# Performance work log

Measured on AMD Instinct MI355X. Metric: run time of the kernel, lower is better.

Reference implementation:

```python
import jax, jax.numpy as jnp
import numpy as np

EPS = 1e-5


def causal_conv(x, w, b):
    # x: [B,C,N,T], w: [O,C,K] (temporal kernel), b: [O]; left-pad time by K-1 (causal)
    K = w.shape[-1]
    y = jax.lax.conv_general_dilated(
        x, w[:, :, None, :], window_strides=(1, 1),
        padding=[(0, 0), (K - 1, 0)],
        dimension_numbers=('NCHW', 'OIHW', 'NCHW'))
    return y + b[None, :, None, None]


def batchnorm(x, gamma, beta):
    # training-mode BatchNorm2d: stats over (B, N, T) per channel
    m = x.mean(axis=(0, 2, 3), keepdims=True)
    v = x.var(axis=(0, 2, 3), keepdims=True)
    return (x - m) * jax.lax.rsqrt(v + EPS) * gamma[None, :, None, None] + beta[None, :, None, None]


def st_layer(x, supports, gamma, beta, rw, rb, aw, ab, gw, gb, ow, ob):
    # residual 1x1 conv
    res = jnp.einsum('bcnt,oc->bont', x, rw) + rb[None, :, None, None]
    x = jax.nn.relu(batchnorm(x, gamma, beta))
    aff = causal_conv(x, aw, ab)
    gate = causal_conv(x, gw, gb)
    x = jnp.tanh(aff + res) * jax.nn.sigmoid(gate)
    B, C, N, T = x.shape
    hs = jnp.einsum('bcvt,evw->becwt', x, supports)  # [B,E,C,N,T]
    full = jnp.concatenate([x, hs.reshape(B, -1, N, T)], axis=1)  # [B,C*(E+1),N,T]
    return jnp.einsum('bcnt,oc->bont', full, ow) + ob[None, :, None, None]


def reference(x, supports, bn_gamma, bn_beta, res_w, res_b, aff_w, aff_b,
              gate_w, gate_b, gc_w, gc_b, attn_w1, attn_b1, attn_w2, attn_b2,
              attn_w3, attn_b3):
    L = bn_gamma.shape[0]
    h = x
    stack = [x]
    for i in range(L):
        h = st_layer(h, supports, bn_gamma[i], bn_beta[i], res_w[i], res_b[i],
                     aff_w[i], aff_b[i], gate_w[i], gate_b[i], gc_w[i], gc_b[i])
        stack.append(h)
    xs = jax.nn.relu(jnp.stack(stack, axis=2))  # [B,C,L+1,N,T]
    # SelfAttention: 1x1x1 conv3d chain C->64->64->1 with ReLU after first two
    e = jax.nn.relu(jnp.einsum('bclnt,oc->bolnt', xs, attn_w1) + attn_b1[None, :, None, None, None])
    e = jax.nn.relu(jnp.einsum('bclnt,oc->bolnt', e, attn_w2) + attn_b2[None, :, None, None, None])
    e = jnp.einsum('bclnt,oc->bolnt', e, attn_w3) + attn_b3[None, :, None, None, None]  # [B,1,L+1,N,T]
    w = jax.nn.softmax(e, axis=2)
    out = (xs * w).sum(axis=2)  # [B,C,N,T]
    return out


def setup_inputs() -> dict:
    B, C, N, T = 16, 32, 500, 64
    L, E, K, D = 4, 2, 3, 64
    key = jax.random.key(0)
    ks = jax.random.split(key, 20)
    s = 0.1
    return {
        'x': jax.random.normal(ks[0], (B, C, N, T), jnp.float32),
        'supports': jax.random.uniform(ks[1], (E, N, N), jnp.float32) / N,
        'bn_gamma': jnp.ones((L, C), jnp.float32),
        'bn_beta': jnp.zeros((L, C), jnp.float32),
        'res_w': jax.random.normal(ks[2], (L, C, C), jnp.float32) * s,
        'res_b': jax.random.normal(ks[3], (L, C), jnp.float32) * s,
        'aff_w': jax.random.normal(ks[4], (L, C, C, K), jnp.float32) * s,
        'aff_b': jax.random.normal(ks[5], (L, C), jnp.float32) * s,
        'gate_w': jax.random.normal(ks[6], (L, C, C, K), jnp.float32) * s,
        'gate_b': jax.random.normal(ks[7], (L, C), jnp.float32) * s,
        'gc_w': jax.random.normal(ks[8], (L, C, C * (E + 1)), jnp.float32) * s,
        'gc_b': jax.random.normal(ks[9], (L, C), jnp.float32) * s,
        'attn_w1': jax.random.normal(ks[10], (D, C), jnp.float32) * s,
        'attn_b1': jax.random.normal(ks[11], (D,), jnp.float32) * s,
        'attn_w2': jax.random.normal(ks[12], (D, D), jnp.float32) * s,
        'attn_b2': jax.random.normal(ks[13], (D,), jnp.float32) * s,
        'attn_w3': jax.random.normal(ks[14], (1, D), jnp.float32) * s,
        'attn_b3': jax.random.normal(ks[15], (1,), jnp.float32) * s,
    }
```

## Files before the change

### kernel.cpp

```cpp
#include <hip/hip_runtime.h>
#include <hip/hip_bf16.h>
#include <math.h>

#define B_ 16
#define C_ 32
#define N_ 500
#define T_ 64
#define L_ 4
#define BSTR (C_*N_*T_)
#define CSTR (N_*T_)
#define TENS ((size_t)B_*C_*N_*T_)
#define CNT_ 512000.0

typedef short s8v __attribute__((ext_vector_type(8)));
typedef float f4v __attribute__((ext_vector_type(4)));
typedef unsigned short u16;

__global__ __launch_bounds__(256) void zero_kernel(double* __restrict__ p,
                                                   float* __restrict__ slack) {
  p[threadIdx.x] = 0.0;
  if (threadIdx.x < 16) slack[threadIdx.x] = 0.f;
}

__global__ __launch_bounds__(256) void stats_kernel(const float* __restrict__ h,
                                                    double* __restrict__ st) {
  int c = blockIdx.x, b = blockIdx.y, tid = threadIdx.x;
  const float4* p = (const float4*)(h + (size_t)b*BSTR + (size_t)c*CSTR);
  double s = 0.0, s2 = 0.0;
  for (int i = tid; i < CSTR/4; i += 256) {
    float4 v = p[i];
    s  += (double)v.x + (double)v.y + (double)v.z + (double)v.w;
    s2 += (double)v.x*v.x + (double)v.y*v.y + (double)v.z*v.z + (double)v.w*v.w;
  }
  __shared__ double sd[256], sd2[256];
  sd[tid] = s; sd2[tid] = s2; __syncthreads();
  for (int off = 128; off > 0; off >>= 1) {
    if (tid < off) { sd[tid] += sd[tid+off]; sd2[tid] += sd2[tid+off]; }
    __syncthreads();
  }
  if (tid == 0) { atomicAdd(&st[2*c], sd[0]); atomicAdd(&st[2*c+1], sd2[0]); }
}

__global__ __launch_bounds__(256) void aconv_kernel(const float* __restrict__ sup,
                                                    short* __restrict__ ATh) {
  int idx = blockIdx.x*256 + threadIdx.x;
  int k = idx & 1023, w = idx >> 10;
  float val = 0.f;
  if (k < 1000 && w < N_) {
    int s = k >= 500;
    int v = k - s*500;
    val = sup[((size_t)s*N_ + v)*N_ + w];
  }
  __hip_bfloat16 bh = __float2bfloat16(val);
  ATh[idx] = *(short*)&bh;
}

__global__ __launch_bounds__(256) void w1t_kernel(const float* __restrict__ W1,
                                                  float* __restrict__ W1T) {
  int idx = blockIdx.x*256 + threadIdx.x;
  int c = idx >> 6, k = idx & 63;
  W1T[c*64 + k] = W1[k*32 + c];
}

__global__ __launch_bounds__(256) void wprep_kernel(
    const float* __restrict__ aw, const float* __restrict__ gw,
    const float* __restrict__ rw,
    u16* __restrict__ wagh, u16* __restrict__ wagl,
    u16* __restrict__ wrh,  u16* __restrict__ wrl)
{
  int idx = blockIdx.x*256 + threadIdx.x;
  if (idx >= 28672) return;
  float v; u16 *dh, *dl; int di;
  if (idx < 24576) {
    int l = idx / 6144, r = idx % 6144;
    int tap = r / 2048, col = (r >> 5) & 63, c = r & 31;
    v = (col < 32) ? aw[l*3072 + (col*32 + c)*3 + tap]
                   : gw[l*3072 + ((col-32)*32 + c)*3 + tap];
    dh = wagh; dl = wagl; di = idx;
  } else {
    int j = idx - 24576;
    int l = j >> 10, o = (j >> 5) & 31, c = j & 31;
    v = rw[l*1024 + o*32 + c];
    dh = wrh; dl = wrl; di = j;
  }
  __hip_bfloat16 bh = __float2bfloat16(v);
  float fh = __bfloat162float(bh);
  __hip_bfloat16 bl = __float2bfloat16(v - fh);
  dh[di] = *(u16*)&bh;
  dl[di] = *(u16*)&bl;
}

__global__ __launch_bounds__(512) void fuse4_kernel(
    const float* __restrict__ h, const double* __restrict__ st,
    const float* __restrict__ gamma, const float* __restrict__ beta,
    const u16* __restrict__ wagh, const u16* __restrict__ wagl,
    const u16* __restrict__ wrh,  const u16* __restrict__ wrl,
    const float* __restrict__ rb, const float* __restrict__ ab,
    const float* __restrict__ gb,
    const float* __restrict__ gcw, const float* __restrict__ gcb,
    float* __restrict__ Y0, u16* __restrict__ Y1h, u16* __restrict__ Y2h)
{
  __shared__ __align__(16) char smem[41600];
  __shared__ float ssc[C_], ssb[C_];
  u16* Sxh = (u16*)smem;
  u16* Sxl = Sxh + 5280;
  u16* Shh = Sxl + 5280;
  u16* Shl = Shh + 5120;
  float* Sz = (float*)smem;

  int tid = threadIdx.x;
  int bx  = blockIdx.x;
  int b = bx / 250, np = bx - b*250;
  size_t off0 = (size_t)b*BSTR + (size_t)(np*2)*T_;

  int m  = tid & 127;
  int c0 = (tid >> 7) << 3;
  float hv[8];
  #pragma unroll
  for (int j = 0; j < 8; j++)
    hv[j] = h[off0 + (size_t)(c0 + j)*CSTR + m];

  if (tid < C_) {
    double mm = st[2*tid] * (1.0/CNT_);
    double vv = st[2*tid+1] * (1.0/CNT_) - mm*mm;
    float sc = gamma[tid] * (float)(1.0 / sqrt(vv + 1e-5));
    ssc[tid] = sc;
    ssb[tid] = beta[tid] - (float)mm * sc;
  }
  __syncthreads();

  union P { u16 s[8]; int4 v; };
  P hh8, hl8, xh8, xl8;
  #pragma unroll
  for (int j = 0; j < 8; j++) {
    float hval = hv[j];
    __hip_bfloat16 t1 = __float2bfloat16(hval);
    hh8.s[j] = *(u16*)&t1;
    __hip_bfloat16 t2 = __float2bfloat16(hval - __bfloat162float(t1));
    hl8.s[j] = *(u16*)&t2;
    float xval = fmaxf(fmaf(hval, ssc[c0+j], ssb[c0+j]), 0.f);
    __hip_bfloat16 t3 = __float2bfloat16(xval);
    xh8.s[j] = *(u16*)&t3;
    __hip_bfloat16 t4 = __float2bfloat16(xval - __bfloat162float(t3));
    xl8.s[j] = *(u16*)&t4;
  }
  *(int4*)&Shh[m*40 + c0] = hh8.v;
  *(int4*)&Shl[m*40 + c0] = hl8.v;
  int xrow = m + 2 + (m >> 6)*2;
  *(int4*)&Sxh[xrow*40 + c0] = xh8.v;
  *(int4*)&Sxl[xrow*40 + c0] = xl8.v;
  if (tid < 32) {
    int pl = tid >> 4, rsel = (tid >> 2) & 3, ch = tid & 3;
    int row = (rsel & 1) + (rsel >> 1)*66;
    int4 z4 = {0,0,0,0};
    *(int4*)((pl ? Sxl : Sxh) + row*40 + ch*8) = z4;
  }
  __syncthreads();

  int lane = tid & 63;
  int wave = __builtin_amdgcn_readfirstlane(tid >> 6);
  int node = wave >> 2, t0 = (wave & 3) << 4;
  int l15 = lane & 15, q = lane >> 4;

  f4v affc[2], gatec[2], resc[2];
  #pragma unroll
  for (int i = 0; i < 2; i++) {
    affc[i] = (f4v){0.f,0.f,0.f,0.f};
    gatec[i] = (f4v){0.f,0.f,0.f,0.f};
    resc[i] = (f4v){0.f,0.f,0.f,0.f};
  }

  {
    int ha = (node*64 + t0 + l15)*40 + q*8;
    s8v hhf = *(const s8v*)&Shh[ha];
    s8v hlf = *(const s8v*)&Shl[ha];
    #pragma unroll
    for (int ct = 0; ct < 2; ct++) {
      int wb = (ct*16 + l15)*32 + q*8;
      s8v wh = *(const s8v*)&wrh[wb];
      s8v wl = *(const s8v*)&wrl[wb];
      f4v d = resc[ct];
      d = __builtin_amdgcn_mfma_f32_16x16x32_bf16(hhf, wh, d, 0, 0, 0);
      d = __builtin_amdgcn_mfma_f32_16x16x32_bf16(hlf, wh, d, 0, 0, 0);
      d = __builtin_amdgcn_mfma_f32_16x16x32_bf16(hhf, wl, d, 0, 0, 0);
      resc[ct] = d;
    }
  }
  #pragma unroll
  for (int tap = 0; tap < 3; tap++) {
    int xa = (node*66 + t0 + l15 + tap)*40 + q*8;
    s8v xhf = *(const s8v*)&Sxh[xa];
    s8v xlf = *(const s8v*)&Sxl[xa];
    #pragma unroll
    for (int ct = 0; ct < 4; ct++) {
      int wb = (tap*64 + ct*16 + l15)*32 + q*8;
      s8v wh = *(const s8v*)&wagh[wb];
      s8v wl = *(const s8v*)&wagl[wb];
      f4v d = (ct < 2) ? affc[ct] : gatec[ct-2];
      d = __builtin_amdgcn_mfma_f32_16x16x32_bf16(xhf, wh, d, 0, 0, 0);
      d = __builtin_amdgcn_mfma_f32_16x16x32_bf16(xlf, wh, d, 0, 0, 0);
      d = __builtin_amdgcn_mfma_f32_16x16x32_bf16(xhf, wl, d, 0, 0, 0);
      if (ct < 2) affc[ct] = d; else gatec[ct-2] = d;
    }
  }
  __syncthreads();

  #pragma unroll
  for (int ct = 0; ct < 2; ct++) {
    int o = ct*16 + l15;
    float abias = ab[o] + rb[o];
    float gbias = gb[o];
    #pragma unroll
    for (int r = 0; r < 4; r++) {
      float a = affc[ct][r] + resc[ct][r] + abias;
      float g = gatec[ct][r] + gbias;
      float z = tanhf(a) * (1.f/(1.f + expf(-g)));
      Sz[node*2080 + o*65 + (t0 + q*4 + r)] = z;
    }
  }
  __syncthreads();

  int t = tid & 63;
  int og = wave;
  float y0a[2][4] = {}, y1a[2][4] = {}, y2a[2][4] = {};
  for (int c = 0; c < C_; c++) {
    float g0[4], g1[4], g2[4];
    #pragma unroll
    for (int jq = 0; jq < 4; jq++) {
      const float* gr = gcw + (og*4 + jq)*96;
      g0[jq] = gr[c]; g1[jq] = gr[32 + c]; g2[jq] = gr[64 + c];
    }
    #pragma unroll
    for (int nn = 0; nn < 2; nn++) {
      float zc = Sz[nn*2080 + c*65 + t];
      #pragma unroll
      for (int jq = 0; jq < 4; jq++) {
        y0a[nn][jq] = fmaf(g0[jq], zc, y0a[nn][jq]);
        y1a[nn][jq] = fmaf(g1[jq], zc, y1a[nn][jq]);
        y2a[nn][jq] = fmaf(g2[jq], zc, y2a[nn][jq]);
      }
    }
  }
  #pragma unroll
  for (int nn = 0; nn < 2; nn++)
    #pragma unroll
    for (int jq = 0; jq < 4; jq++) {
      int oo = og*4 + jq;
      size_t pp = off0 + (size_t)nn*T_ + (size_t)oo*CSTR + t;
      Y0[pp] = y0a[nn][jq] + gcb[oo];
      __hip_bfloat16 b1 = __float2bfloat16(y1a[nn][jq]);
      __hip_bfloat16 b2 = __float2bfloat16(y2a[nn][jq]);
      Y1h[pp] = *(u16*)&b1;
      Y2h[pp] = *(u16*)&b2;
    }
}

__global__ __launch_bounds__(256) void trans_kernel(
    const u16* __restrict__ Y1h, const u16* __restrict__ Y2h,
    u16* __restrict__ Yt)
{
  __shared__ u16 S[64*68];
  int bx = blockIdx.x;
  int o = bx & 31, vg = bx >> 5;
  int b = blockIdx.y;
  int tid = threadIdx.x;
  u16* dst = Yt + (size_t)(b*C_ + o)*64000;
  for (int ic = 0; ic < 4; ic++) {
    int vc = vg*4 + ic;
    __syncthreads();
    #pragma unroll
    for (int i = 0; i < 2; i++) {
      int vrow = (tid >> 3) + i*32;
      int vv = vc*64 + vrow;
      int t8 = (tid & 7)*8;
      int4 val = {0,0,0,0};
      if (vv < 1000) {
        int sup = vv >= 500;
        int n = vv - sup*500;
        const u16* src = (sup ? Y2h : Y1h) + (size_t)b*BSTR + (size_t)o*CSTR
                         + (size_t)n*T_;
        val = *(const int4*)(src + t8);
      }
      *(int4*)&S[vrow*68 + t8] = val;
    }
    __syncthreads();
    int t2 = tid >> 3, vs = tid & 7;
    if (vc < 15 || vs < 5) {
      unsigned r[8];
      #pragma unroll
      for (int j = 0; j < 8; j++)
        r[j] = *(const unsigned*)&S[(vs*8 + j)*68 + 2*t2];
      u16 lo[8], hi[8];
      #pragma unroll
      for (int j = 0; j < 8; j++) { lo[j] = (u16)r[j]; hi[j] = (u16)(r[j] >> 16); }
      *(int4*)(dst + (size_t)(2*t2)*1000   + vc*64 + vs*8) = *(const int4*)lo;
      *(int4*)(dst + (size_t)(2*t2+1)*1000 + vc*64 + vs*8) = *(const int4*)hi;
    }
  }
}

__global__ __launch_bounds__(256) void diff6_kernel(
    const u16* __restrict__ Yt,
    const short* __restrict__ ATh,
    float* __restrict__ out, double* __restrict__ stp)
{
  __shared__ short Asd[64*40];
  __shared__ short Bsd[128*40];

  int tid = threadIdx.x;
  int bx = blockIdx.x;
  int mtile = bx & 15, wtile = bx >> 4;
  int b = blockIdx.y;
  int w0 = wtile << 6;

  int lane = tid & 63;
  int wave = __builtin_amdgcn_readfirstlane(tid >> 6);
  int wi = wave & 1, wj = wave >> 1;
  int l15 = lane & 15, quad = lane >> 4;
  int o = mtile*2 + wj;

  int offA[2], offB[4];
  #pragma unroll
  for (int ti = 0; ti < 2; ti++) offA[ti] = (wi*32 + ti*16 + l15)*40 + quad*8;
  #pragma unroll
  for (int tj = 0; tj < 4; tj++) offB[tj] = (wj*64 + tj*16 + l15)*40 + quad*8;

  int akq = tid & 3, awl = tid >> 2;
  const short* aSrc = ATh + (size_t)(w0 + awl)*1024 + akq*8;
  short* aDst = &Asd[awl*40 + akq*8];
  const u16* bSrc[2]; short* bDst[2];
  #pragma unroll
  for (int i = 0; i < 2; i++) {
    int idx = tid + i*256;
    int kq = idx & 3, m = idx >> 2;
    int oo = m >> 6, tl = m & 63;
    bSrc[i] = Yt + ((size_t)(b*C_ + mtile*2 + oo)*64 + tl)*1000 + kq*8;
    bDst[i] = &Bsd[m*40 + kq*8];
  }

  f4v acc[8];
  #pragma unroll
  for (int i = 0; i < 8; i++) acc[i] = (f4v){0.f, 0.f, 0.f, 0.f};

  for (int k0 = 0; k0 < 1024; k0 += 32) {
    __syncthreads();
    *(int4*)aDst    = *(const int4*)(aSrc    + k0);
    *(int4*)bDst[0] = *(const int4*)(bSrc[0] + k0);
    *(int4*)bDst[1] = *(const int4*)(bSrc[1] + k0);
    __syncthreads();
    s8v bv[4];
    #pragma unroll
    for (int tj = 0; tj < 4; tj++) bv[tj] = *(const s8v*)&Bsd[offB[tj]];
    #pragma unroll
    for (int ti = 0; ti < 2; ti++) {
      s8v av = *(const s8v*)&Asd[offA[ti]];
      #pragma unroll
      for (int tj = 0; tj < 4; tj++)
        acc[ti*4+tj] = __builtin_amdgcn_mfma_f32_16x16x32_bf16(
                           av, bv[tj], acc[ti*4+tj], 0, 0, 0);
    }
  }

  float s = 0.f, s2 = 0.f;
  #pragma unroll
  for (int tj = 0; tj < 4; tj++) {
    int t = tj*16 + l15;
    float* obase = out + (((size_t)b*C_ + o)*N_)*T_ + t;
    #pragma unroll
    for (int ti = 0; ti < 2; ti++) {
      int wbase = w0 + wi*32 + ti*16 + quad*4;
      #pragma unroll
      for (int r = 0; r < 4; r++) {
        int w = wbase + r;
        if (w < N_) {
          float* p = obase + (size_t)w*T_;
          float val = *p + acc[ti*4+tj][r];
          *p = val;
          s += val;
          s2 = fmaf(val, val, s2);
        }
      }
    }
  }
  if (stp) {
    #pragma unroll
    for (int d = 32; d > 0; d >>= 1) {
      s  += __shfl_down(s,  d, 64);
      s2 += __shfl_down(s2, d, 64);
    }
    if (lane == 0) {
      atomicAdd(&stp[2*o],     (double)s);
      atomicAdd(&stp[2*o + 1], (double)s2);
    }
  }
}

__global__ __launch_bounds__(256) void attn3_kernel(
    const float* __restrict__ hsrc, float* __restrict__ O,
    float* __restrict__ sden,
    const float* __restrict__ W1T, const float* __restrict__ b1,
    const float* __restrict__ W2, const float* __restrict__ b2,
    const float* __restrict__ w3, const float* __restrict__ b3,
    int init)
{
  int tid = threadIdx.x;
  int t = tid & 63;
  int g = __builtin_amdgcn_readfirstlane(tid >> 6);
  int bx = blockIdx.x;
  int b = bx / 125;
  int n = (bx - b*125)*4 + g;
  size_t off = (size_t)b*BSTR + (size_t)n*T_;

  float h1r[64];
  #pragma unroll
  for (int k = 0; k < 64; k++) h1r[k] = b1[k];
  for (int c = 0; c < C_; c++) {
    float xv = fmaxf(hsrc[off + (size_t)c*CSTR + t], 0.f);
    const float* wr = W1T + c*64;
    #pragma unroll
    for (int k = 0; k < 64; k++) h1r[k] = fmaf(wr[k], xv, h1r[k]);
  }
  #pragma unroll
  for (int k = 0; k < 64; k++) h1r[k] = fmaxf(h1r[k], 0.f);

  float e = b3[0];
  for (int j = 0; j < 64; j++) {
    const float* w2r = W2 + j*64;
    float a0 = 0.f, a1 = 0.f, a2 = 0.f, a3 = 0.f;
    #pragma unroll
    for (int i = 0; i < 64; i += 4) {
      a0 = fmaf(w2r[i+0], h1r[i+0], a0);
      a1 = fmaf(w2r[i+1], h1r[i+1], a1);
      a2 = fmaf(w2r[i+2], h1r[i+2], a2);
      a3 = fmaf(w2r[i+3], h1r[i+3], a3);
    }
    float a = b2[j] + ((a0+a1)+(a2+a3));
    e = fmaf(w3[j], fmaxf(a, 0.f), e);
  }
  float p = expf(e);

  size_t si = (size_t)b*CSTR + (size_t)n*T_ + t;
  float so = init ? 0.f : sden[si];
  sden[si] = so + p;

  for (int c = 0; c < C_; c++) {
    size_t pi = off + (size_t)c*CSTR + t;
    float xv = fmaxf(hsrc[pi], 0.f);
    float ov = init ? 0.f : O[pi];
    O[pi] = fmaf(p, xv, ov);
  }
}

__global__ __launch_bounds__(256) void norm_kernel(float* __restrict__ O,
                                                   const float* __restrict__ sden) {
  unsigned idx = (blockIdx.x*256u + threadIdx.x) * 4u;
  unsigned b = idx / BSTR;
  unsigned r = idx - b*BSTR;
  unsigned nt = r % CSTR;
  float4 o = *(float4*)(O + idx);
  const float* sp = sden + (size_t)b*CSTR + nt;
  o.x /= sp[0]; o.y /= sp[1]; o.z /= sp[2]; o.w /= sp[3];
  *(float4*)(O + idx) = o;
}

extern "C" void kernel_launch(void* const* d_in, const int* in_sizes, int n_in,
                              void* d_out, int out_size, void* d_ws, size_t ws_size,
                              hipStream_t stream)
{
  const float* x    = (const float*)d_in[0];
  const float* sup  = (const float*)d_in[1];
  const float* bng  = (const float*)d_in[2];
  const float* bnb  = (const float*)d_in[3];
  const float* rw   = (const float*)d_in[4];
  const float* rb   = (const float*)d_in[5];
  const float* aw   = (const float*)d_in[6];
  const float* ab   = (const float*)d_in[7];
  const float* gw   = (const float*)d_in[8];
  const float* gb   = (const float*)d_in[9];
  const float* gcw  = (const float*)d_in[10];
  const float* gcb  = (const float*)d_in[11];
  const float* w1   = (const float*)d_in[12];
  const float* ab1  = (const float*)d_in[13];
  const float* w2   = (const float*)d_in[14];
  const float* ab2  = (const float*)d_in[15];
  const float* w3   = (const float*)d_in[16];
  const float* ab3  = (const float*)d_in[17];
  float* out = (float*)d_out;

  float* ws   = (float*)d_ws;
  float* bufA = ws;
  u16*   Y1h  = (u16*)(ws + TENS);
  u16*   Y2h  = Y1h + TENS;
  u16*   Yt   = (u16*)(ws + (size_t)2*TENS);
  float* slack= ws + (size_t)2*TENS + 16384000;
  float* sden = slack + 16;
  double* st  = (double*)(sden + (size_t)B_*N_*T_);
  short* ATh  = (short*)((float*)st + 1024);
  float* W1T  = (float*)(ATh + (size_t)512*1024);
  u16* WAGh = (u16*)(W1T + 2048);
  u16* WAGl = WAGh + 24576;
  u16* WRh  = WAGl + 24576;
  u16* WRl  = WRh + 4096;

  zero_kernel<<<1, 256, 0, stream>>>(st, slack);
  aconv_kernel<<<2048, 256, 0, stream>>>(sup, ATh);
  w1t_kernel<<<8, 256, 0, stream>>>(w1, W1T);
  wprep_kernel<<<112, 256, 0, stream>>>(aw, gw, rw, WAGh, WAGl, WRh, WRl);
  stats_kernel<<<dim3(C_, B_), 256, 0, stream>>>(x, st);
  attn3_kernel<<<B_*125, 256, 0, stream>>>(x, out, sden, W1T, ab1, w2, ab2, w3, ab3, 1);

  const float* hcur = x;
  for (int l = 0; l < L_; l++) {
    fuse4_kernel<<<B_*250, 512, 0, stream>>>(
        hcur, st + l*64, bng + l*C_, bnb + l*C_,
        WAGh + l*6144, WAGl + l*6144, WRh + l*1024, WRl + l*1024,
        rb + l*C_, ab + l*C_, gb + l*C_,
        gcw + l*C_*96, gcb + l*C_,
        bufA, Y1h, Y2h);
    trans_kernel<<<dim3(128, B_), 256, 0, stream>>>(Y1h, Y2h, Yt);
    diff6_kernel<<<dim3(128, B_), 256, 0, stream>>>(
        Yt, ATh, bufA, (l < L_-1) ? (st + (l+1)*64) : nullptr);
    attn3_kernel<<<B_*125, 256, 0, stream>>>(bufA, out, sden, W1T, ab1, w2, ab2, w3, ab3, 0);
    hcur = bufA;
  }
  norm_kernel<<<16000, 256, 0, stream>>>(out, sden);
}
```

Baseline: 1.638 ms.

## Move attention MLP onto bf16 MFMA with LDS staging

Rewrites the attention scoring kernel so the C->64->64 1x1 convolutions run as bf16 16x16x32 MFMA tiles. Activations are staged through LDS per wave instead of each thread holding a 64-float hidden vector and doing scalar FMAs. The activations are also kept in registers, so the second global read of the input for the weighted sum goes away. The weight prep kernel gains bf16 conversion of W1/W2 and replaces the transpose kernel. This trades fp32 precision in the attention logits for bf16 and relies on tensor-core throughput.

```diff
diff --git a/kernel.cpp b/kernel.cpp
--- a/kernel.cpp
+++ b/kernel.cpp
@@ -55,21 +55,27 @@
   ATh[idx] = *(short*)&bh;
 }
 
-__global__ __launch_bounds__(256) void w1t_kernel(const float* __restrict__ W1,
-                                                  float* __restrict__ W1T) {
-  int idx = blockIdx.x*256 + threadIdx.x;
-  int c = idx >> 6, k = idx & 63;
-  W1T[c*64 + k] = W1[k*32 + c];
-}
-
 __global__ __launch_bounds__(256) void wprep_kernel(
     const float* __restrict__ aw, const float* __restrict__ gw,
     const float* __restrict__ rw,
+    const float* __restrict__ w1, const float* __restrict__ w2,
     u16* __restrict__ wagh, u16* __restrict__ wagl,
-    u16* __restrict__ wrh,  u16* __restrict__ wrl)
+    u16* __restrict__ wrh,  u16* __restrict__ wrl,
+    u16* __restrict__ W1bf, u16* __restrict__ W2bf)
 {
   int idx = blockIdx.x*256 + threadIdx.x;
-  if (idx >= 28672) return;
+  if (idx >= 34816) return;
+  if (idx >= 28672) {
+    int j = idx - 28672;
+    if (j < 2048) {
+      __hip_bfloat16 bv = __float2bfloat16(w1[j]);
+      W1bf[j] = *(u16*)&bv;
+    } else {
+      __hip_bfloat16 bv = __float2bfloat16(w2[j - 2048]);
+      W2bf[j - 2048] = *(u16*)&bv;
+    }
+    return;
+  }
   float v; u16 *dh, *dl; int di;
   if (idx < 24576) {
     int l = idx / 6144, r = idx % 6144;
@@ -395,59 +401,122 @@
   }
 }
 
-__global__ __launch_bounds__(256) void attn3_kernel(
+__global__ __launch_bounds__(256) void attn4_kernel(
     const float* __restrict__ hsrc, float* __restrict__ O,
     float* __restrict__ sden,
-    const float* __restrict__ W1T, const float* __restrict__ b1,
-    const float* __restrict__ W2, const float* __restrict__ b2,
+    const u16* __restrict__ W1bf, const float* __restrict__ b1,
+    const u16* __restrict__ W2bf, const float* __restrict__ b2,
     const float* __restrict__ w3, const float* __restrict__ b3,
     int init)
 {
+  __shared__ u16 Sh[4*4608];
+  __shared__ float Se[4*64];
+
   int tid = threadIdx.x;
-  int t = tid & 63;
-  int g = __builtin_amdgcn_readfirstlane(tid >> 6);
+  int lane = tid & 63;
+  int wave = __builtin_amdgcn_readfirstlane(tid >> 6);
   int bx = blockIdx.x;
   int b = bx / 125;
-  int n = (bx - b*125)*4 + g;
+  int n = (bx - b*125)*4 + wave;
   size_t off = (size_t)b*BSTR + (size_t)n*T_;
-
-  float h1r[64];
-  #pragma unroll
-  for (int k = 0; k < 64; k++) h1r[k] = b1[k];
-  for (int c = 0; c < C_; c++) {
-    float xv = fmaxf(hsrc[off + (size_t)c*CSTR + t], 0.f);
-    const float* wr = W1T + c*64;
-    #pragma unroll
-    for (int k = 0; k < 64; k++) h1r[k] = fmaf(wr[k], xv, h1r[k]);
-  }
-  #pragma unroll
-  for (int k = 0; k < 64; k++) h1r[k] = fmaxf(h1r[k], 0.f);
-
-  float e = b3[0];
-  for (int j = 0; j < 64; j++) {
-    const float* w2r = W2 + j*64;
-    float a0 = 0.f, a1 = 0.f, a2 = 0.f, a3 = 0.f;
-    #pragma unroll
-    for (int i = 0; i < 64; i += 4) {
-      a0 = fmaf(w2r[i+0], h1r[i+0], a0);
-      a1 = fmaf(w2r[i+1], h1r[i+1], a1);
-      a2 = fmaf(w2r[i+2], h1r[i+2], a2);
-      a3 = fmaf(w2r[i+3], h1r[i+3], a3);
-    }
-    float a = b2[j] + ((a0+a1)+(a2+a3));
-    e = fmaf(w3[j], fmaxf(a, 0.f), e);
-  }
-  float p = expf(e);
-
-  size_t si = (size_t)b*CSTR + (size_t)n*T_ + t;
+  int l15 = lane & 15, q = lane >> 4;
+
+  u16* R = Sh + wave*4608;
+  float* Ew = Se + wave*64;
+
+  float xv[32];
+  #pragma unroll 8
+  for (int c = 0; c < 32; c++)
+    xv[c] = fmaxf(hsrc[off + (size_t)c*CSTR + lane], 0.f);
+  #pragma unroll
+  for (int c8 = 0; c8 < 4; c8++) {
+    union { u16 s[8]; int4 v; } pk;
+    #pragma unroll
+    for (int j = 0; j < 8; j++) {
+      __hip_bfloat16 bv = __float2bfloat16(xv[c8*8 + j]);
+      pk.s[j] = *(u16*)&bv;
+    }
+    *(int4*)&R[lane*40 + c8*8] = pk.v;
+  }
+
+  f4v c1[4][4];
+  {
+    s8v a1[4];
+    #pragma unroll
+    for (int mt = 0; mt < 4; mt++)
+      a1[mt] = *(const s8v*)&R[(mt*16 + l15)*40 + q*8];
+    #pragma unroll
+    for (int jt = 0; jt < 4; jt++) {
+      s8v w1f = *(const s8v*)&W1bf[(jt*16 + l15)*32 + q*8];
+      #pragma unroll
+      for (int mt = 0; mt < 4; mt++) {
+        f4v z = (f4v){0.f, 0.f, 0.f, 0.f};
+        c1[mt][jt] = __builtin_amdgcn_mfma_f32_16x16x32_bf16(a1[mt], w1f, z, 0, 0, 0);
+      }
+    }
+  }
+  #pragma unroll
+  for (int jt = 0; jt < 4; jt++) {
+    float bb = b1[jt*16 + l15];
+    #pragma unroll
+    for (int mt = 0; mt < 4; mt++)
+      #pragma unroll
+      for (int r = 0; r < 4; r++) {
+        float v = fmaxf(c1[mt][jt][r] + bb, 0.f);
+        __hip_bfloat16 bv = __float2bfloat16(v);
+        R[(mt*16 + q*4 + r)*72 + jt*16 + l15] = *(u16*)&bv;
+      }
+  }
+  f4v c2[4][4];
+  #pragma unroll
+  for (int mt = 0; mt < 4; mt++)
+    #pragma unroll
+    for (int jt = 0; jt < 4; jt++) c2[mt][jt] = (f4v){0.f, 0.f, 0.f, 0.f};
+  #pragma unroll
+  for (int ks = 0; ks < 2; ks++) {
+    s8v a2[4];
+    #pragma unroll
+    for (int mt = 0; mt < 4; mt++)
+      a2[mt] = *(const s8v*)&R[(mt*16 + l15)*72 + ks*32 + q*8];
+    #pragma unroll
+    for (int jt = 0; jt < 4; jt++) {
+      s8v w2f = *(const s8v*)&W2bf[(jt*16 + l15)*64 + ks*32 + q*8];
+      #pragma unroll
+      for (int mt = 0; mt < 4; mt++)
+        c2[mt][jt] = __builtin_amdgcn_mfma_f32_16x16x32_bf16(a2[mt], w2f, c2[mt][jt], 0, 0, 0);
+    }
+  }
+  float pe[4][4] = {};
+  #pragma unroll
+  for (int jt = 0; jt < 4; jt++) {
+    float bb = b2[jt*16 + l15];
+    float ww = w3[jt*16 + l15];
+    #pragma unroll
+    for (int mt = 0; mt < 4; mt++)
+      #pragma unroll
+      for (int r = 0; r < 4; r++)
+        pe[mt][r] = fmaf(ww, fmaxf(c2[mt][jt][r] + bb, 0.f), pe[mt][r]);
+  }
+  #pragma unroll
+  for (int msk = 1; msk < 16; msk <<= 1)
+    #pragma unroll
+    for (int mt = 0; mt < 4; mt++)
+      #pragma unroll
+      for (int r = 0; r < 4; r++)
+        pe[mt][r] += __shfl_xor(pe[mt][r], msk, 64);
+  #pragma unroll
+  for (int i = 0; i < 16; i++)
+    if (l15 == i)
+      Ew[(i >> 2)*16 + q*4 + (i & 3)] = pe[i >> 2][i & 3];
+  float p = expf(Ew[lane] + b3[0]);
+  size_t si = (size_t)b*CSTR + (size_t)n*T_ + lane;
   float so = init ? 0.f : sden[si];
   sden[si] = so + p;
-
-  for (int c = 0; c < C_; c++) {
-    size_t pi = off + (size_t)c*CSTR + t;
-    float xv = fmaxf(hsrc[pi], 0.f);
+  #pragma unroll 8
+  for (int c = 0; c < 32; c++) {
+    size_t pi = off + (size_t)c*CSTR + lane;
     float ov = init ? 0.f : O[pi];
-    O[pi] = fmaf(p, xv, ov);
+    O[pi] = fmaf(p, xv[c], ov);
   }
 }
 
@@ -496,18 +565,19 @@
   float* sden = slack + 16;
   double* st  = (double*)(sden + (size_t)B_*N_*T_);
   short* ATh  = (short*)((float*)st + 1024);
-  float* W1T  = (float*)(ATh + (size_t)512*1024);
-  u16* WAGh = (u16*)(W1T + 2048);
+  u16* WAGh = (u16*)(ATh + (size_t)512*1024);
   u16* WAGl = WAGh + 24576;
   u16* WRh  = WAGl + 24576;
   u16* WRl  = WRh + 4096;
+  u16* W1bf = WRl + 4096;
+  u16* W2bf = W1bf + 2048;
 
   zero_kernel<<<1, 256, 0, stream>>>(st, slack);
   aconv_kernel<<<2048, 256, 0, stream>>>(sup, ATh);
-  w1t_kernel<<<8, 256, 0, stream>>>(w1, W1T);
-  wprep_kernel<<<112, 256, 0, stream>>>(aw, gw, rw, WAGh, WAGl, WRh, WRl);
+  wprep_kernel<<<136, 256, 0, stream>>>(aw, gw, rw, w1, w2,
+                                        WAGh, WAGl, WRh, WRl, W1bf, W2bf);
   stats_kernel<<<dim3(C_, B_), 256, 0, stream>>>(x, st);
-  attn3_kernel<<<B_*125, 256, 0, stream>>>(x, out, sden, W1T, ab1, w2, ab2, w3, ab3, 1);
+  attn4_kernel<<<B_*125, 256, 0, stream>>>(x, out, sden, W1bf, ab1, W2bf, ab2, w3, ab3, 1);
 
   const float* hcur = x;
   for (int l = 0; l < L_; l++) {
@@ -520,7 +590,7 @@
     trans_kernel<<<dim3(128, B_), 256, 0, stream>>>(Y1h, Y2h, Yt);
     diff6_kernel<<<dim3(128, B_), 256, 0, stream>>>(
         Yt, ATh, bufA, (l < L_-1) ? (st + (l+1)*64) : nullptr);
-    attn3_kernel<<<B_*125, 256, 0, stream>>>(bufA, out, sden, W1T, ab1, w2, ab2, w3, ab3, 0);
+    attn4_kernel<<<B_*125, 256, 0, stream>>>(bufA, out, sden, W1bf, ab1, W2bf, ab2, w3, ab3, 0);
     hcur = bufA;
   }
   norm_kernel<<<16000, 256, 0, stream>>>(out, sden);
```

After: 1.582 ms. 3.4% less time.
